# Optimization experiments

Hardware: AMD Instinct MI355X
Metric: run time of the kernel (lower is better)

## Reference

```python
import jax, jax.numpy as jnp
import numpy as np

RES_V, RES_H = 16, 32
N_SAMPLES = 100
GRID = 256
N_CH = 11  # 3 color + 1 alpha + 3 w + 1 lamb + 3 s


def setup_inputs() -> dict:
    key = jax.random.key(0)
    k1, = jax.random.split(key, 1)
    SGLV = jax.random.uniform(k1, (N_CH, GRID, GRID, GRID), dtype=jnp.float32)
    origin = jnp.zeros((3,), dtype=jnp.float32)  # box center -> all rays hit
    voxel_range = jnp.array([[-1.0, -1.0, -1.0], [1.0, 1.0, 1.0]], dtype=jnp.float32)
    return {"origin": origin, "SGLV": SGLV, "voxel_range": voxel_range}


def _trilerp_zeros(vol, pts):
    # vol: [C, D, H, W]; pts: [..., 3] normalized coords, x->W, y->H, z->D.
    # Matches F.grid_sample(mode='bilinear', align_corners=True, padding_mode='zeros').
    C, D, H, W = vol.shape
    lead = pts.shape[:-1]
    p = pts.reshape(-1, 3)
    ix = (p[:, 0] + 1.0) * 0.5 * (W - 1)
    iy = (p[:, 1] + 1.0) * 0.5 * (H - 1)
    iz = (p[:, 2] + 1.0) * 0.5 * (D - 1)
    x0f = jnp.floor(ix); y0f = jnp.floor(iy); z0f = jnp.floor(iz)
    fx = ix - x0f; fy = iy - y0f; fz = iz - z0f
    x0 = x0f.astype(jnp.int32); y0 = y0f.astype(jnp.int32); z0 = z0f.astype(jnp.int32)
    vol_f = vol.reshape(C, -1)

    def corner(xi, yi, zi, wgt):
        valid = ((xi >= 0) & (xi < W) & (yi >= 0) & (yi < H) & (zi >= 0) & (zi < D))
        xc = jnp.clip(xi, 0, W - 1)
        yc = jnp.clip(yi, 0, H - 1)
        zc = jnp.clip(zi, 0, D - 1)
        lin = (zc * H + yc) * W + xc
        v = vol_f[:, lin]  # [C, N]
        return v * (wgt * valid.astype(wgt.dtype))[None, :]

    out = (corner(x0,     y0,     z0,     (1 - fx) * (1 - fy) * (1 - fz))
         + corner(x0 + 1, y0,     z0,     fx       * (1 - fy) * (1 - fz))
         + corner(x0,     y0 + 1, z0,     (1 - fx) * fy       * (1 - fz))
         + corner(x0 + 1, y0 + 1, z0,     fx       * fy       * (1 - fz))
         + corner(x0,     y0,     z0 + 1, (1 - fx) * (1 - fy) * fz)
         + corner(x0 + 1, y0,     z0 + 1, fx       * (1 - fy) * fz)
         + corner(x0,     y0 + 1, z0 + 1, (1 - fx) * fy       * fz)
         + corner(x0 + 1, y0 + 1, z0 + 1, fx       * fy       * fz))
    return out.reshape((C,) + lead)


def _envmap_directions():
    v = jnp.arange(RES_V, dtype=jnp.float32)
    u = jnp.arange(RES_H, dtype=jnp.float32)
    v_grid, u_grid = jnp.meshgrid(v, u, indexing='ij')
    phi = 2.0 * jnp.pi * u_grid / RES_H
    theta = jnp.pi * v_grid / RES_V
    st = jnp.sin(theta)
    dirs = jnp.stack([st * jnp.cos(phi), jnp.cos(theta), st * jnp.sin(phi)], axis=-1)
    n = jnp.linalg.norm(dirs, axis=-1, keepdims=True)
    return dirs / jnp.maximum(n, 1e-12)  # [16, 32, 3]


def _ray_box(origin, dirs, voxel_range):
    inf = jnp.float32(jnp.inf)
    zero = dirs == 0.0
    d_safe = jnp.where(zero, 1.0, dirs)  # double-where trick: keeps grads finite

    def slab(bound):
        num = bound - origin  # broadcast [3] -> [16,32,3]
        num = jnp.broadcast_to(num, dirs.shape)
        return jnp.where(zero, jnp.where(num > 0, inf, -inf), num / d_safe)

    t_min = slab(voxel_range[0])
    t_max = slab(voxel_range[1])
    t0 = jnp.min(jnp.where(t_min > 0, t_min, inf), axis=-1)
    t1 = jnp.min(jnp.where(t_max > 0, t_max, inf), axis=-1)
    t_start = jnp.zeros_like(t0)
    t_end = jnp.minimum(t0, t1)
    return t_start, t_end


def reference(origin, SGLV, voxel_range):
    dirs = _envmap_directions()                       # [16,32,3]
    t_start, t_end = _ray_box(origin, dirs, voxel_range)  # [16,32] each
    lin = jnp.linspace(0.0, 1.0, N_SAMPLES, dtype=jnp.float32)
    ts = t_start[..., None] + lin * (t_end - t_start)[..., None]   # [16,32,100]
    points = origin + ts[..., None] * dirs[:, :, None, :]          # [16,32,100,3]
    npts = (points - voxel_range[0]) / (voxel_range[1] - voxel_range[0]) * 2.0 - 1.0
    samp = _trilerp_zeros(SGLV, npts)                 # [11,16,32,100]
    alpha = samp[3]                                   # [16,32,100]
    transmittance = jnp.cumprod(1.0 - alpha + 1e-10, axis=-1)
    weights = alpha * transmittance                   # [16,32,100]
    acc = jnp.sum(weights[None] * samp, axis=-1)      # [11,16,32]
    acc_c, acc_w, acc_lamb, acc_s = acc[:3], acc[4:7], acc[7], acc[8:]
    s_dot_dir = jnp.einsum('vuk,kvu->vu', dirs, acc_s)  # [16,32]
    envmap = acc_c + acc_w * jnp.exp(acc_lamb * (s_dot_dir - 1.0))
    return envmap  # [3,16,32]
```

## Files before the change

kernel.cpp:

```cpp
#include <hip/hip_runtime.h>

#define RES_V 16
#define RES_H 32
#define NS    100
#define GRD   256
#define NCH   11
#define BLK   256
#define SPECN 16
#define EPS   1e-5f

__device__ __forceinline__ int iclamp(int x, int lo, int hi) {
    return x < lo ? lo : (x > hi ? hi : x);
}

__device__ __forceinline__ float corner_reduce(float x) {
    x += __shfl_xor(x, 1, 64);
    x += __shfl_xor(x, 2, 64);
    x += __shfl_xor(x, 4, 64);
    return x;
}

__device__ __forceinline__ float group_scan(float fac, int lane) {
    float p = fac;
    #pragma unroll
    for (int off = 8; off < 64; off <<= 1) {
        float o = __shfl_up(p, off, 64);
        if (lane >= off) p *= o;
    }
    return p;
}

__global__ __launch_bounds__(BLK) void sglv_render_kernel(
    const float* __restrict__ origin,
    const float* __restrict__ SGLV,
    const float* __restrict__ vrange,
    float* __restrict__ out)
{
    const int ray    = blockIdx.x;
    const int v      = ray >> 5;
    const int u      = ray & 31;
    const int tid    = threadIdx.x;
    const int lane   = tid & 63;
    const int wid    = tid >> 6;
    const int sg     = tid >> 3;
    const int corner = tid & 7;

    __shared__ float s_wtot[4];
    __shared__ float s_red[4][NCH];

    const float PIF = 3.14159265358979323846f;
    float phi   = (2.0f * PIF / (float)RES_H) * (float)u;
    float theta = (PIF / (float)RES_V) * (float)v;
    float stv = sinf(theta);
    float dx0 = stv * cosf(phi);
    float dy0 = cosf(theta);
    float dz0 = stv * sinf(phi);
    float nrm = sqrtf(dx0 * dx0 + dy0 * dy0 + dz0 * dz0);
    nrm = fmaxf(nrm, 1e-12f);
    float d[3] = { dx0 / nrm, dy0 / nrm, dz0 / nrm };

    float org[3] = { origin[0], origin[1], origin[2] };
    float vr0[3] = { vrange[0], vrange[1], vrange[2] };
    float vr1[3] = { vrange[3], vrange[4], vrange[5] };

    const float INF = __builtin_inff();
    float t0 = INF, t1 = INF;
    #pragma unroll
    for (int k = 0; k < 3; ++k) {
        float num0 = vr0[k] - org[k];
        float num1 = vr1[k] - org[k];
        float tmin, tmax;
        if (d[k] == 0.0f) {
            tmin = (num0 > 0.0f) ? INF : -INF;
            tmax = (num1 > 0.0f) ? INF : -INF;
        } else {
            tmin = num0 / d[k];
            tmax = num1 / d[k];
        }
        t0 = fminf(t0, (tmin > 0.0f) ? tmin : INF);
        t1 = fminf(t1, (tmax > 0.0f) ? tmax : INF);
    }
    float t_end   = fminf(t0, t1);
    float t_start = 0.0f;

    const size_t CS = (size_t)GRD * GRD * GRD;

    float acc[NCH];
    #pragma unroll
    for (int c = 0; c < NCH; ++c) acc[c] = 0.0f;
    float running_T = 1.0f;

    for (int s0 = 0; s0 < NS; s0 += 32) {
        const int  s   = s0 + sg;
        const bool act = (s < NS);

        float  w = 0.0f;
        size_t base = 0;
        if (act) {
            float lin = (float)s / (float)(NS - 1);
            float t = t_start + lin * (t_end - t_start);
            float np_[3];
            #pragma unroll
            for (int k = 0; k < 3; ++k) {
                float p = org[k] + t * d[k];
                np_[k] = (p - vr0[k]) / (vr1[k] - vr0[k]) * 2.0f - 1.0f;
            }
            float ix = (np_[0] + 1.0f) * 0.5f * (float)(GRD - 1);
            float iy = (np_[1] + 1.0f) * 0.5f * (float)(GRD - 1);
            float iz = (np_[2] + 1.0f) * 0.5f * (float)(GRD - 1);
            float x0f = floorf(ix), y0f = floorf(iy), z0f = floorf(iz);
            float fx = ix - x0f, fy = iy - y0f, fz = iz - z0f;
            int x0 = (int)x0f, y0 = (int)y0f, z0 = (int)z0f;
            int cx = corner & 1, cy = (corner >> 1) & 1, cz = corner >> 2;
            int xi = x0 + cx, yi = y0 + cy, zi = z0 + cz;
            w = (cx ? fx : 1.0f - fx)
              * (cy ? fy : 1.0f - fy)
              * (cz ? fz : 1.0f - fz);
            bool valid = ((unsigned)xi < GRD) & ((unsigned)yi < GRD)
                       & ((unsigned)zi < GRD);
            w = valid ? w : 0.0f;
            int xc = iclamp(xi, 0, GRD - 1);
            int yc = iclamp(yi, 0, GRD - 1);
            int zc = iclamp(zi, 0, GRD - 1);
            base = ((size_t)zc * GRD + (size_t)yc) * GRD + (size_t)xc;
        }

        float part[NCH];
        #pragma unroll
        for (int c = 0; c < NCH; ++c) part[c] = 0.0f;
        const bool spec = (s0 == 0) && (s < SPECN);
        if (act) {
            if (spec) {
                #pragma unroll
                for (int c = 0; c < NCH; ++c)
                    part[c] = w * SGLV[(size_t)c * CS + base];
            } else {
                part[3] = w * SGLV[3 * CS + base];
            }
        }

        float alpha = corner_reduce(part[3]);
        float fac = act ? (1.0f - alpha) + 1e-10f : 1.0f;
        float p = group_scan(fac, lane);
        if (lane == 63) s_wtot[wid] = p;
        __syncthreads();

        float pre = running_T;
        for (int w2 = 0; w2 < wid; ++w2) pre *= s_wtot[w2];
        float chunk_prod = s_wtot[0] * s_wtot[1] * s_wtot[2] * s_wtot[3];
        float T   = pre * p;
        float wgt = act ? alpha * T : 0.0f;
        const bool live = act && (T > EPS);

        if (live && !spec) {
            #pragma unroll
            for (int c = 0; c < NCH; ++c) {
                if (c == 3) continue;
                part[c] = w * SGLV[(size_t)c * CS + base];
            }
        }

        #pragma unroll
        for (int c = 0; c < NCH; ++c) {
            if (c == 3) continue;
            acc[c] += wgt * part[c];
        }

        running_T *= chunk_prod;
        __syncthreads();
        if (running_T <= EPS) break;
    }

    #pragma unroll
    for (int c = 0; c < NCH; ++c) {
        if (c == 3) continue;
        float val = acc[c];
        #pragma unroll
        for (int off = 32; off > 0; off >>= 1)
            val += __shfl_xor(val, off, 64);
        if (lane == 0) s_red[wid][c] = val;
    }
    __syncthreads();

    if (tid == 0) {
        float a[NCH];
        #pragma unroll
        for (int c = 0; c < NCH; ++c) {
            if (c == 3) { a[c] = 0.0f; continue; }
            a[c] = s_red[0][c] + s_red[1][c] + s_red[2][c] + s_red[3][c];
        }
        float sdd = d[0] * a[8] + d[1] * a[9] + d[2] * a[10];
        float e = expf(a[7] * (sdd - 1.0f));
        int pix = v * RES_H + u;
        out[0 * RES_V * RES_H + pix] = a[0] + a[4] * e;
        out[1 * RES_V * RES_H + pix] = a[1] + a[5] * e;
        out[2 * RES_V * RES_H + pix] = a[2] + a[6] * e;
    }
}

extern "C" void kernel_launch(void* const* d_in, const int* in_sizes, int n_in,
                              void* d_out, int out_size, void* d_ws, size_t ws_size,
                              hipStream_t stream) {
    const float* origin = (const float*)d_in[0];
    const float* SGLV   = (const float*)d_in[1];
    const float* vrange = (const float*)d_in[2];
    float* out = (float*)d_out;

    sglv_render_kernel<<<dim3(RES_V * RES_H), dim3(BLK), 0, stream>>>(
        origin, SGLV, vrange, out);
}
```

Before: 14.01 us.

## Split channel gathers across two thread halves per sample with 512-thread blocks

Doubles the block to 512 threads so each sample-corner pair is handled by two threads. One half fetches alpha plus color and channel 4, the other fetches the remaining six channels, which roughly halves the serial gathers per thread. Alpha is shared between the halves by shuffle, and the final reductions are adjusted to match. The cost is more threads, more waves to synchronise per block, and extra shuffle work.

```diff
diff --git a/kernel.cpp b/kernel.cpp
--- a/kernel.cpp
+++ b/kernel.cpp
@@ -5,29 +5,12 @@
 #define NS    100
 #define GRD   256
 #define NCH   11
-#define BLK   256
+#define BLK   512
 #define SPECN 16
 #define EPS   1e-5f
 
 __device__ __forceinline__ int iclamp(int x, int lo, int hi) {
     return x < lo ? lo : (x > hi ? hi : x);
-}
-
-__device__ __forceinline__ float corner_reduce(float x) {
-    x += __shfl_xor(x, 1, 64);
-    x += __shfl_xor(x, 2, 64);
-    x += __shfl_xor(x, 4, 64);
-    return x;
-}
-
-__device__ __forceinline__ float group_scan(float fac, int lane) {
-    float p = fac;
-    #pragma unroll
-    for (int off = 8; off < 64; off <<= 1) {
-        float o = __shfl_up(p, off, 64);
-        if (lane >= off) p *= o;
-    }
-    return p;
 }
 
 __global__ __launch_bounds__(BLK) void sglv_render_kernel(
@@ -42,11 +25,16 @@
     const int tid    = threadIdx.x;
     const int lane   = tid & 63;
     const int wid    = tid >> 6;
-    const int sg     = tid >> 3;
     const int corner = tid & 7;
-
-    __shared__ float s_wtot[4];
-    __shared__ float s_red[4][NCH];
+    const int h      = (tid >> 3) & 1;
+    const int sg     = tid >> 4;
+
+    __shared__ float s_wtot[8];
+    __shared__ float s_red[8][NCH];
+
+    const int chA[5] = {3, 0, 1, 2, 4};
+    const int chB[6] = {5, 6, 7, 8, 9, 10};
+    const int nmine  = h ? 6 : 5;
 
     const float PIF = 3.14159265358979323846f;
     float phi   = (2.0f * PIF / (float)RES_H) * (float)u;
@@ -85,9 +73,9 @@
 
     const size_t CS = (size_t)GRD * GRD * GRD;
 
-    float acc[NCH];
+    float accL[6];
     #pragma unroll
-    for (int c = 0; c < NCH; ++c) acc[c] = 0.0f;
+    for (int i = 0; i < 6; ++i) accL[i] = 0.0f;
     float running_T = 1.0f;
 
     for (int s0 = 0; s0 < NS; s0 += 32) {
@@ -125,46 +113,67 @@
             base = ((size_t)zc * GRD + (size_t)yc) * GRD + (size_t)xc;
         }
 
-        float part[NCH];
-        #pragma unroll
-        for (int c = 0; c < NCH; ++c) part[c] = 0.0f;
+        float part[6];
+        #pragma unroll
+        for (int i = 0; i < 6; ++i) part[i] = 0.0f;
         const bool spec = (s0 == 0) && (s < SPECN);
         if (act) {
             if (spec) {
-                #pragma unroll
-                for (int c = 0; c < NCH; ++c)
-                    part[c] = w * SGLV[(size_t)c * CS + base];
-            } else {
-                part[3] = w * SGLV[3 * CS + base];
+                if (h == 0) {
+                    #pragma unroll
+                    for (int i = 0; i < 5; ++i)
+                        part[i] = w * SGLV[(size_t)chA[i] * CS + base];
+                } else {
+                    #pragma unroll
+                    for (int i = 0; i < 6; ++i)
+                        part[i] = w * SGLV[(size_t)chB[i] * CS + base];
+                }
+            } else if (h == 0) {
+                part[0] = w * SGLV[3 * CS + base];
             }
         }
 
-        float alpha = corner_reduce(part[3]);
+        float alpha = part[0];
+        alpha += __shfl_xor(alpha, 1, 64);
+        alpha += __shfl_xor(alpha, 2, 64);
+        alpha += __shfl_xor(alpha, 4, 64);
+        float aswap = __shfl_xor(alpha, 8, 64);
+        alpha = h ? aswap : alpha;
+
         float fac = act ? (1.0f - alpha) + 1e-10f : 1.0f;
-        float p = group_scan(fac, lane);
+        float p = fac;
+        {
+            float o = __shfl_up(p, 16, 64); if (lane >= 16) p *= o;
+            o       = __shfl_up(p, 32, 64); if (lane >= 32) p *= o;
+        }
         if (lane == 63) s_wtot[wid] = p;
         __syncthreads();
 
         float pre = running_T;
         for (int w2 = 0; w2 < wid; ++w2) pre *= s_wtot[w2];
-        float chunk_prod = s_wtot[0] * s_wtot[1] * s_wtot[2] * s_wtot[3];
+        float chunk_prod = s_wtot[0] * s_wtot[1] * s_wtot[2] * s_wtot[3]
+                         * s_wtot[4] * s_wtot[5] * s_wtot[6] * s_wtot[7];
         float T   = pre * p;
         float wgt = act ? alpha * T : 0.0f;
         const bool live = act && (T > EPS);
 
         if (live && !spec) {
-            #pragma unroll
-            for (int c = 0; c < NCH; ++c) {
-                if (c == 3) continue;
-                part[c] = w * SGLV[(size_t)c * CS + base];
+            const int start = (h == 0) ? 1 : 0;
+            if (h == 0) {
+                #pragma unroll
+                for (int i = 1; i < 5; ++i)
+                    part[i] = w * SGLV[(size_t)chA[i] * CS + base];
+            } else {
+                #pragma unroll
+                for (int i = 0; i < 6; ++i)
+                    part[i] = w * SGLV[(size_t)chB[i] * CS + base];
             }
-        }
-
-        #pragma unroll
-        for (int c = 0; c < NCH; ++c) {
-            if (c == 3) continue;
-            acc[c] += wgt * part[c];
-        }
+            (void)start;
+        }
+
+        #pragma unroll
+        for (int i = 0; i < 6; ++i)
+            accL[i] += wgt * part[i];
 
         running_T *= chunk_prod;
         __syncthreads();
@@ -172,13 +181,22 @@
     }
 
     #pragma unroll
-    for (int c = 0; c < NCH; ++c) {
-        if (c == 3) continue;
-        float val = acc[c];
-        #pragma unroll
-        for (int off = 32; off > 0; off >>= 1)
-            val += __shfl_xor(val, off, 64);
-        if (lane == 0) s_red[wid][c] = val;
+    for (int i = 0; i < 6; ++i) {
+        float val = accL[i];
+        val += __shfl_xor(val, 1, 64);
+        val += __shfl_xor(val, 2, 64);
+        val += __shfl_xor(val, 4, 64);
+        val += __shfl_xor(val, 16, 64);
+        val += __shfl_xor(val, 32, 64);
+        accL[i] = val;
+    }
+    if (lane == 0) {
+        #pragma unroll
+        for (int i = 0; i < 5; ++i) s_red[wid][chA[i]] = accL[i];
+    }
+    if (lane == 8) {
+        #pragma unroll
+        for (int i = 0; i < 6; ++i) s_red[wid][chB[i]] = accL[i];
     }
     __syncthreads();
 
@@ -186,8 +204,10 @@
         float a[NCH];
         #pragma unroll
         for (int c = 0; c < NCH; ++c) {
-            if (c == 3) { a[c] = 0.0f; continue; }
-            a[c] = s_red[0][c] + s_red[1][c] + s_red[2][c] + s_red[3][c];
+            float x = 0.0f;
+            #pragma unroll
+            for (int w2 = 0; w2 < 8; ++w2) x += s_red[w2][c];
+            a[c] = x;
         }
         float sdd = d[0] * a[8] + d[1] * a[9] + d[2] * a[10];
         float e = expf(a[7] * (sdd - 1.0f));
```

Result: no change. 13.98 us (-0.3%).
